# Performance work log

Measured on AMD Instinct MI355X. Metric: run time of the kernel, lower is better.

## Reference

```python
import jax, jax.numpy as jnp
import numpy as np

WIN_LEN = 3072
HOP = 192


def hann_window(n):
    # torch.hann_window(n, periodic=False)
    k = jnp.arange(n, dtype=jnp.float32)
    return 0.5 - 0.5 * jnp.cos(2.0 * jnp.pi * k / (n - 1))


def setup_inputs() -> dict:
    key = jax.random.key(0)
    k1, k2 = jax.random.split(key)
    B, C, F, T = 8, 1, 128, 1000
    filter_bands = jax.random.uniform(k1, (B, C, F, T), dtype=jnp.float32)
    # torch: rand*2-1 uniform in [-1, 1)
    noise = jax.random.uniform(k2, (B, C, (T - 1) * HOP), dtype=jnp.float32) * 2.0 - 1.0
    return {"filter_bands": filter_bands, "noise": noise}


def reference(filter_bands, noise):
    B, C, F, T = filter_bands.shape
    half = WIN_LEN // 2  # 1536
    padded = jnp.pad(noise, ((0, 0), (0, 0), (half, half)))
    L = padded.shape[-1]  # (T-1)*HOP + 2*half
    # unfold: [T, WIN_LEN] gather indices, frames [B, C, T, WIN_LEN]
    frame_idx = jnp.arange(T)[:, None] * HOP + jnp.arange(WIN_LEN)[None, :]
    frames = padded[:, :, frame_idx]
    # nearest interpolation of bands F -> half (torch 'nearest': floor(i*F/out))
    src = (jnp.arange(half) * F) // half
    filt = filter_bands[:, :, src, :]          # [B, C, half, T]
    filt = jnp.transpose(filt, (0, 1, 3, 2))   # [B, C, T, half]
    filt = jnp.pad(filt, ((0, 0), (0, 0), (0, 0), (1, 0)))  # prepend DC zero -> half+1 bins
    spec = jnp.fft.rfft(frames)                # [B, C, T, half+1] complex
    out_frames = jnp.fft.irfft(filt * spec, n=WIN_LEN)  # [B, C, T, WIN_LEN]
    out_frames = out_frames * hann_window(WIN_LEN)
    # overlap-add (F.fold with stride HOP)
    out = jnp.zeros((B, C, L), dtype=out_frames.dtype)
    out = out.at[:, :, frame_idx.reshape(-1)].add(out_frames.reshape(B, C, -1))
    return out[:, :, half:-half]
```

## Files before the change

kernel.cpp:

```cpp
#include <hip/hip_runtime.h>

#define NFFT 3072
#define THREADS 256
#define HOP 192
#define HALF 1536
#define TFRAMES 1000
#define OUTLEN 191808
#define NBANDS 128
#define PI_F 3.14159265358979323846f

__device__ __forceinline__ float2 cadd(float2 a,float2 b){return make_float2(a.x+b.x,a.y+b.y);}
__device__ __forceinline__ float2 csub(float2 a,float2 b){return make_float2(a.x-b.x,a.y-b.y);}
__device__ __forceinline__ float2 cmul(float2 a,float2 b){
    return make_float2(fmaf(a.x,b.x,-a.y*b.y), fmaf(a.x,b.y,a.y*b.x));
}
__device__ __forceinline__ float2 cmuln_i(float2 a){return make_float2(a.y,-a.x);}
__device__ __forceinline__ float2 cneg(float2 a){return make_float2(-a.x,-a.y);}

__device__ __forceinline__ int IDX(int i){ return i + (i>>4); }

__device__ __forceinline__ void dft4(float2 a0,float2 a1,float2 a2,float2 a3,
                                     float2&y0,float2&y1,float2&y2,float2&y3){
    float2 e0=cadd(a0,a2), e1=csub(a0,a2), o0=cadd(a1,a3), o1=csub(a1,a3);
    y0=cadd(e0,o0); y2=csub(e0,o0);
    float2 io=make_float2(-o1.y,o1.x);
    y1=csub(e1,io); y3=cadd(e1,io);
}
__device__ __forceinline__ void dft3(float2 a0,float2 a1,float2 a2,
                                     float2&y0,float2&y1,float2&y2){
    float2 s=cadd(a1,a2), d=csub(a1,a2);
    y0=cadd(a0,s);
    float2 t=make_float2(a0.x-0.5f*s.x, a0.y-0.5f*s.y);
    const float S3=0.86602540378443864676f;
    float2 id=make_float2(S3*d.y,-S3*d.x);
    y1=cadd(t,id); y2=csub(t,id);
}

__device__ __forceinline__ void dft12(float2 a[12], float2 o[12]){
    float2 u[3][4];
    #pragma unroll
    for(int n2=0;n2<3;++n2)
        dft4(a[n2],a[3+n2],a[6+n2],a[9+n2],u[n2][0],u[n2][1],u[n2][2],u[n2][3]);
    const float2 W1=make_float2( 0.86602540378443865f,-0.5f);
    const float2 W2=make_float2( 0.5f,-0.86602540378443865f);
    const float2 W4=make_float2(-0.5f,-0.86602540378443865f);
    u[1][1]=cmul(u[1][1],W1); u[1][2]=cmul(u[1][2],W2); u[1][3]=cmuln_i(u[1][3]);
    u[2][1]=cmul(u[2][1],W2); u[2][2]=cmul(u[2][2],W4); u[2][3]=cneg(u[2][3]);
    #pragma unroll
    for(int k1=0;k1<4;++k1)
        dft3(u[0][k1],u[1][k1],u[2][k1], o[k1],o[k1+4],o[k1+8]);
}

__device__ __forceinline__ void dft16(float2 a[16], float2 o[16]){
    float2 u[4][4];
    #pragma unroll
    for(int n2=0;n2<4;++n2)
        dft4(a[n2],a[4+n2],a[8+n2],a[12+n2],u[n2][0],u[n2][1],u[n2][2],u[n2][3]);
    const float C16=0.92387953251128674f, S16=0.38268343236508977f, R2=0.70710678118654752f;
    const float2 W1=make_float2( C16,-S16), W2=make_float2( R2,-R2), W3=make_float2( S16,-C16);
    const float2 W6=make_float2(-R2,-R2),  W9=make_float2(-C16, S16);
    u[1][1]=cmul(u[1][1],W1); u[1][2]=cmul(u[1][2],W2);   u[1][3]=cmul(u[1][3],W3);
    u[2][1]=cmul(u[2][1],W2); u[2][2]=cmuln_i(u[2][2]);   u[2][3]=cmul(u[2][3],W6);
    u[3][1]=cmul(u[3][1],W3); u[3][2]=cmul(u[3][2],W6);   u[3][3]=cmul(u[3][3],W9);
    #pragma unroll
    for(int k1=0;k1<4;++k1)
        dft4(u[0][k1],u[1][k1],u[2][k1],u[3][k1], o[k1],o[k1+4],o[k1+8],o[k1+12]);
}

template<int R>
__device__ __forceinline__ void twiddle_pows(float2* o, float ang){
    float s,c; __sincosf(ang,&s,&c);
    float2 w1=make_float2(c,s);
    float2 w2=cmul(w1,w1);
    float2 w3=cmul(w2,w1);
    float2 w4=cmul(w2,w2);
    o[1]=cmul(o[1],w1); o[2]=cmul(o[2],w2); o[3]=cmul(o[3],w3);
    float2 w8=cmul(w4,w4);
    float2 w5=cmul(w4,w1), w6=cmul(w4,w2), w7=cmul(w4,w3);
    o[4]=cmul(o[4],w4); o[5]=cmul(o[5],w5); o[6]=cmul(o[6],w6); o[7]=cmul(o[7],w7);
    float2 w9=cmul(w8,w1), w10=cmul(w8,w2), w11=cmul(w8,w3);
    o[8]=cmul(o[8],w8); o[9]=cmul(o[9],w9); o[10]=cmul(o[10],w10); o[11]=cmul(o[11],w11);
    if constexpr (R>12){
        float2 w12=cmul(w8,w4), w13=cmul(w8,w5), w14=cmul(w8,w6), w15=cmul(w8,w7);
        o[12]=cmul(o[12],w12); o[13]=cmul(o[13],w13); o[14]=cmul(o[14],w14); o[15]=cmul(o[15],w15);
    }
}

__device__ __forceinline__ void stageB(float2* A, int tid){
    const bool act = tid < 192;
    float2 o[16];
    int q=0,p=0;
    if(act){
        q = tid % 12; p = tid / 12;
        float2 a[16];
        int ib = IDX(q + 12*p);
        #pragma unroll
        for(int l=0;l<16;++l) a[l] = A[ib + 204*l];
        dft16(a,o);
        twiddle_pows<16>(o, -2.0f*PI_F*(float)p*(1.0f/256.0f));
    }
    __syncthreads();
    if(act){
        #pragma unroll
        for(int j=0;j<16;++j) A[IDX(q + 192*p + 12*j)] = o[j];
    }
    __syncthreads();
}

__global__ __launch_bounds__(THREADS,4)
void filtered_noise_kernel(const float* __restrict__ fb,
                           const float* __restrict__ noise,
                           float* __restrict__ out)
{
    __shared__ float2 A[NFFT + NFFT/16];
    __shared__ float gf[2*NBANDS];

    const int tid = threadIdx.x;
    const int wg  = blockIdx.x;
    const int b   = wg / (TFRAMES/2);
    const int tp  = wg % (TFRAMES/2);
    const int t0  = 2*tp;
    const float* nz = noise + (size_t)b * OUTLEN;
    const int base0 = t0*HOP - HALF;

    gf[tid] = fb[((size_t)b*NBANDS + (tid & 127))*TFRAMES + t0 + (tid >> 7)];

    {
        float2 a[12], o[12];
        #pragma unroll
        for(int l=0;l<12;++l){
            int i0 = base0 + tid + 256*l;
            float x0 = (i0 >= 0 && i0 < OUTLEN) ? nz[i0] : 0.0f;
            int i1 = i0 + HOP;
            float x1 = (i1 >= 0 && i1 < OUTLEN) ? nz[i1] : 0.0f;
            a[l] = make_float2(x0, x1);
        }
        dft12(a,o);
        twiddle_pows<12>(o, -2.0f*PI_F*(float)tid*(1.0f/3072.0f));
        #pragma unroll
        for(int j=0;j<12;++j) A[IDX(12*tid + j)] = o[j];
    }
    __syncthreads();

    stageB(A, tid);

    {
        const bool act = tid < 192;
        float2 o[16];
        if(act){
            float2 a[16];
            int ib = IDX(tid);
            #pragma unroll
            for(int l=0;l<16;++l) a[l] = A[ib + 204*l];
            dft16(a,o);
        }
        __syncthreads();
        if(act){
            int ib = IDX(tid);
            #pragma unroll
            for(int j=0;j<16;++j) A[ib + 204*j] = o[j];
        }
        __syncthreads();
    }

    {
        const int p = tid;
        float2 z[12], zm[12];
        {
            int ib = IDX(p);
            #pragma unroll
            for(int l=0;l<12;++l) z[l] = A[ib + 272*l];
        }
        {
            int pm = (p==0) ? 0 : (256 - p);
            int ib = IDX(pm);
            #pragma unroll
            for(int l=0;l<12;++l) zm[l] = A[ib + 272*l];
        }
        float2 w[12];
        #pragma unroll
        for(int l=0;l<12;++l){
            int k = p + 256*l;
            int j = (k <= HALF) ? k : (NFFT - k);
            float aa = 0.0f, bb = 0.0f;
            if(j){
                int band = (j-1)/12;
                float Gx = gf[band], Gy = gf[NBANDS + band];
                aa = 0.5f*(Gx+Gy); bb = 0.5f*(Gx-Gy);
            }
            float2 Zm = (p==0) ? ((l==0) ? z[0] : z[12-l]) : zm[11-l];
            w[l] = make_float2( fmaf(aa, z[l].x,  bb*Zm.x),
                                fmaf(-aa, z[l].y, bb*Zm.y) );
        }
        float2 o[12];
        dft12(w,o);
        twiddle_pows<12>(o, -2.0f*PI_F*(float)p*(1.0f/3072.0f));
        __syncthreads();
        #pragma unroll
        for(int j=0;j<12;++j) A[IDX(12*p + j)] = o[j];
        __syncthreads();
    }

    stageB(A, tid);

    {
        const bool act = tid < 192;
        if(act){
            float2 a[16], o[16];
            int ib = IDX(tid);
            #pragma unroll
            for(int l=0;l<16;++l) a[l] = A[ib + 204*l];
            dft16(a,o);
            const float invN = 1.0f/(float)NFFT;
            float* outb = out + (size_t)b * OUTLEN;
            #pragma unroll
            for(int j=0;j<16;++j){
                int n = tid + 192*j;
                float h = 0.5f - 0.5f*__cosf(2.0f*PI_F*(float)n*(1.0f/3071.0f));
                float s = invN*h;
                float vx =  o[j].x * s;
                float vy = -o[j].y * s;
                int p0 = base0 + n;
                if(p0 >= 0 && p0 < OUTLEN) atomicAdd(&outb[p0], vx);
                int p1 = p0 + HOP;
                if(p1 >= 0 && p1 < OUTLEN) atomicAdd(&outb[p1], vy);
            }
        }
    }
}

extern "C" void kernel_launch(void* const* d_in, const int* in_sizes, int n_in,
                              void* d_out, int out_size, void* d_ws, size_t ws_size,
                              hipStream_t stream)
{
    const float* fb    = (const float*)d_in[0];
    const float* noise = (const float*)d_in[1];
    float* out = (float*)d_out;

    int B = in_sizes[1] / OUTLEN;

    hipMemsetAsync(out, 0, (size_t)out_size * sizeof(float), stream);

    dim3 grid(B * (TFRAMES/2));
    filtered_noise_kernel<<<grid, THREADS, 0, stream>>>(fb, noise, out);
}
```

Measured before the change: 159.4 us.

## Accumulate overlap-add of two frame pairs in shared memory before global atomics

```diff
diff --git a/kernel.cpp b/kernel.cpp
--- a/kernel.cpp
+++ b/kernel.cpp
@@ -8,6 +8,10 @@
 #define OUTLEN 191808
 #define NBANDS 128
 #define PI_F 3.14159265358979323846f
+#define NPAIR 2
+#define NSLOT (2*(NPAIR-1)+17)
+#define CLEN (NSLOT*HOP)
+#define NSB (TFRAMES/(2*NPAIR))
 
 __device__ __forceinline__ float2 cadd(float2 a,float2 b){return make_float2(a.x+b.x,a.y+b.y);}
 __device__ __forceinline__ float2 csub(float2 a,float2 b){return make_float2(a.x-b.x,a.y-b.y);}
@@ -113,98 +117,107 @@
                            float* __restrict__ out)
 {
     __shared__ float2 A[NFFT + NFFT/16];
-    __shared__ float gf[2*NBANDS];
+    __shared__ float  C[CLEN];
 
     const int tid = threadIdx.x;
-    const int wg  = blockIdx.x;
-    const int b   = wg / (TFRAMES/2);
-    const int tp  = wg % (TFRAMES/2);
-    const int t0  = 2*tp;
-    const float* nz = noise + (size_t)b * OUTLEN;
-    const int base0 = t0*HOP - HALF;
-
-    gf[tid] = fb[((size_t)b*NBANDS + (tid & 127))*TFRAMES + t0 + (tid >> 7)];
-
-    {
-        float2 a[12], o[12];
-        #pragma unroll
-        for(int l=0;l<12;++l){
-            int i0 = base0 + tid + 256*l;
-            float x0 = (i0 >= 0 && i0 < OUTLEN) ? nz[i0] : 0.0f;
-            int i1 = i0 + HOP;
-            float x1 = (i1 >= 0 && i1 < OUTLEN) ? nz[i1] : 0.0f;
-            a[l] = make_float2(x0, x1);
-        }
-        dft12(a,o);
-        twiddle_pows<12>(o, -2.0f*PI_F*(float)tid*(1.0f/3072.0f));
-        #pragma unroll
-        for(int j=0;j<12;++j) A[IDX(12*tid + j)] = o[j];
-    }
-    __syncthreads();
-
-    stageB(A, tid);
-
-    {
-        const bool act = tid < 192;
-        float2 o[16];
-        if(act){
-            float2 a[16];
-            int ib = IDX(tid);
-            #pragma unroll
-            for(int l=0;l<16;++l) a[l] = A[ib + 204*l];
-            dft16(a,o);
-        }
+    const int b   = blockIdx.x & 7;
+    const int sb  = blockIdx.x >> 3;
+    const int T0  = sb * (2*NPAIR);
+    const float* nz  = noise + (size_t)b * OUTLEN;
+    const float* fbb = fb + (size_t)b * NBANDS * TFRAMES;
+    const int blockbase = T0*HOP - HALF;
+    const bool act = tid < 192;
+
+    #pragma unroll
+    for(int i=0;i<15;++i){
+        int c = tid + 256*i;
+        if (c < CLEN) C[c] = 0.0f;
+    }
+
+    for(int pi=0; pi<NPAIR; ++pi){
+        const int t0 = T0 + 2*pi;
+        const int base0 = t0*HOP - HALF;
+
         __syncthreads();
-        if(act){
-            int ib = IDX(tid);
-            #pragma unroll
-            for(int j=0;j<16;++j) A[ib + 204*j] = o[j];
+
+        {
+            float2 a[12], o[12];
+            #pragma unroll
+            for(int l=0;l<12;++l){
+                int i0 = base0 + tid + 256*l;
+                float x0 = (i0 >= 0 && i0 < OUTLEN) ? nz[i0] : 0.0f;
+                int i1 = i0 + HOP;
+                float x1 = (i1 >= 0 && i1 < OUTLEN) ? nz[i1] : 0.0f;
+                a[l] = make_float2(x0, x1);
+            }
+            dft12(a,o);
+            twiddle_pows<12>(o, -2.0f*PI_F*(float)tid*(1.0f/3072.0f));
+            #pragma unroll
+            for(int j=0;j<12;++j) A[IDX(12*tid + j)] = o[j];
         }
         __syncthreads();
-    }
-
-    {
-        const int p = tid;
-        float2 z[12], zm[12];
+
+        stageB(A, tid);
+
         {
-            int ib = IDX(p);
-            #pragma unroll
-            for(int l=0;l<12;++l) z[l] = A[ib + 272*l];
-        }
+            float2 o[16];
+            if(act){
+                float2 a[16];
+                int ib = IDX(tid);
+                #pragma unroll
+                for(int l=0;l<16;++l) a[l] = A[ib + 204*l];
+                dft16(a,o);
+            }
+            __syncthreads();
+            if(act){
+                int ib = IDX(tid);
+                #pragma unroll
+                for(int j=0;j<16;++j) A[ib + 204*j] = o[j];
+            }
+            __syncthreads();
+        }
+
         {
-            int pm = (p==0) ? 0 : (256 - p);
-            int ib = IDX(pm);
-            #pragma unroll
-            for(int l=0;l<12;++l) zm[l] = A[ib + 272*l];
-        }
-        float2 w[12];
-        #pragma unroll
-        for(int l=0;l<12;++l){
-            int k = p + 256*l;
-            int j = (k <= HALF) ? k : (NFFT - k);
-            float aa = 0.0f, bb = 0.0f;
-            if(j){
-                int band = (j-1)/12;
-                float Gx = gf[band], Gy = gf[NBANDS + band];
-                aa = 0.5f*(Gx+Gy); bb = 0.5f*(Gx-Gy);
-            }
-            float2 Zm = (p==0) ? ((l==0) ? z[0] : z[12-l]) : zm[11-l];
-            w[l] = make_float2( fmaf(aa, z[l].x,  bb*Zm.x),
-                                fmaf(-aa, z[l].y, bb*Zm.y) );
-        }
-        float2 o[12];
-        dft12(w,o);
-        twiddle_pows<12>(o, -2.0f*PI_F*(float)p*(1.0f/3072.0f));
-        __syncthreads();
-        #pragma unroll
-        for(int j=0;j<12;++j) A[IDX(12*p + j)] = o[j];
-        __syncthreads();
-    }
-
-    stageB(A, tid);
-
-    {
-        const bool act = tid < 192;
+            const int p = tid;
+            float2 z[12], zm[12];
+            {
+                int ib = IDX(p);
+                #pragma unroll
+                for(int l=0;l<12;++l) z[l] = A[ib + 272*l];
+            }
+            {
+                int pm = (p==0) ? 0 : (256 - p);
+                int ib = IDX(pm);
+                #pragma unroll
+                for(int l=0;l<12;++l) zm[l] = A[ib + 272*l];
+            }
+            float2 w[12];
+            #pragma unroll
+            for(int l=0;l<12;++l){
+                int k = p + 256*l;
+                int j = (k <= HALF) ? k : (NFFT - k);
+                float aa = 0.0f, bb = 0.0f;
+                if(j){
+                    int band = (j-1)/12;
+                    float Gx = fbb[band*TFRAMES + t0];
+                    float Gy = fbb[band*TFRAMES + t0 + 1];
+                    aa = 0.5f*(Gx+Gy); bb = 0.5f*(Gx-Gy);
+                }
+                float2 Zm = (p==0) ? ((l==0) ? z[0] : z[12-l]) : zm[11-l];
+                w[l] = make_float2( fmaf(aa, z[l].x,  bb*Zm.x),
+                                    fmaf(-aa, z[l].y, bb*Zm.y) );
+            }
+            float2 o[12];
+            dft12(w,o);
+            twiddle_pows<12>(o, -2.0f*PI_F*(float)p*(1.0f/3072.0f));
+            __syncthreads();
+            #pragma unroll
+            for(int j=0;j<12;++j) A[IDX(12*p + j)] = o[j];
+            __syncthreads();
+        }
+
+        stageB(A, tid);
+
         if(act){
             float2 a[16], o[16];
             int ib = IDX(tid);
@@ -212,19 +225,32 @@
             for(int l=0;l<16;++l) a[l] = A[ib + 204*l];
             dft16(a,o);
             const float invN = 1.0f/(float)NFFT;
-            float* outb = out + (size_t)b * OUTLEN;
-            #pragma unroll
-            for(int j=0;j<16;++j){
-                int n = tid + 192*j;
-                float h = 0.5f - 0.5f*__cosf(2.0f*PI_F*(float)n*(1.0f/3071.0f));
-                float s = invN*h;
-                float vx =  o[j].x * s;
-                float vy = -o[j].y * s;
-                int p0 = base0 + n;
-                if(p0 >= 0 && p0 < OUTLEN) atomicAdd(&outb[p0], vx);
-                int p1 = p0 + HOP;
-                if(p1 >= 0 && p1 < OUTLEN) atomicAdd(&outb[p1], vy);
-            }
+            float vyprev = 0.0f;
+            const int cb = 384*pi + tid;
+            #pragma unroll
+            for(int j=0;j<17;++j){
+                float val = vyprev;
+                if (j < 16){
+                    int n = tid + 192*j;
+                    float h = 0.5f - 0.5f*__cosf(2.0f*PI_F*(float)n*(1.0f/3071.0f));
+                    float s = invN*h;
+                    val   += o[j].x * s;
+                    vyprev = -o[j].y * s;
+                }
+                C[cb + 192*j] += val;
+            }
+        }
+    }
+
+    __syncthreads();
+
+    float* outb = out + (size_t)b * OUTLEN;
+    #pragma unroll
+    for(int i=0;i<15;++i){
+        int c = tid + 256*i;
+        if (c < CLEN){
+            int p = blockbase + c;
+            if (p >= 0 && p < OUTLEN) atomicAdd(&outb[p], C[c]);
         }
     }
 }
@@ -237,10 +263,10 @@
     const float* noise = (const float*)d_in[1];
     float* out = (float*)d_out;
 
-    int B = in_sizes[1] / OUTLEN;
+    const int B = in_sizes[1] / OUTLEN;
 
     hipMemsetAsync(out, 0, (size_t)out_size * sizeof(float), stream);
 
-    dim3 grid(B * (TFRAMES/2));
+    dim3 grid(B * NSB);
     filtered_noise_kernel<<<grid, THREADS, 0, stream>>>(fb, noise, out);
 }
```

Measured after the change: 286.7 us. 1.8x slower.
